# Kernel tuning notes

Hardware: AMD Instinct MI355X
Metric: run time of the kernel (lower is better)

Reference implementation:

```python
import jax, jax.numpy as jnp
import numpy as np

N_NODES = 100000
N_EDGES = 1000000
IN_CH = 64
HID = 64


def setup_inputs() -> dict:
    key = jax.random.key(0)
    ks = jax.random.split(key, 10)
    x = jax.random.normal(ks[0], (N_NODES, IN_CH), dtype=jnp.float32)
    edge_index = jax.random.randint(ks[1], (2, N_EDGES), 0, N_NODES, dtype=jnp.int32)
    s = 1.0 / np.sqrt(IN_CH)
    sh = 1.0 / np.sqrt(HID)
    return {
        "x": x,
        "edge_index": edge_index,
        # conv1: lin_l (applied to aggregated neighbors, has bias), lin_r (self, no bias)
        "w1_l": jax.random.uniform(ks[2], (HID, IN_CH), jnp.float32, -s, s),
        "b1": jnp.zeros((HID,), jnp.float32),
        "w1_r": jax.random.uniform(ks[3], (HID, IN_CH), jnp.float32, -s, s),
        # conv2
        "w2_l": jax.random.uniform(ks[4], (HID, HID), jnp.float32, -sh, sh),
        "b2": jnp.zeros((HID,), jnp.float32),
        "w2_r": jax.random.uniform(ks[5], (HID, HID), jnp.float32, -sh, sh),
        # final linear -> 1
        "w_out": jax.random.uniform(ks[6], (1, HID), jnp.float32, -sh, sh),
        "b_out": jnp.zeros((1,), jnp.float32),
    }


def _sage_conv(x, src, dst, w_l, b, w_r, n_nodes):
    # mean aggregation of source features at destination nodes
    agg = jax.ops.segment_sum(x[src], dst, num_segments=n_nodes)  # [N, d]
    cnt = jax.ops.segment_sum(jnp.ones_like(dst, dtype=x.dtype), dst, num_segments=n_nodes)
    mean = agg / jnp.maximum(cnt, 1.0)[:, None]
    # PyG SAGEConv: lin_l(aggregated) + lin_r(x_self); bias lives in lin_l
    return mean @ w_l.T + b + x @ w_r.T


def reference(x, edge_index, w1_l, b1, w1_r, w2_l, b2, w2_r, w_out, b_out):
    src, dst = edge_index[0], edge_index[1]
    n = x.shape[0]
    h = jax.nn.relu(_sage_conv(x, src, dst, w1_l, b1, w1_r, n))
    h = jax.nn.relu(_sage_conv(h, src, dst, w2_l, b2, w2_r, n))
    logits = h @ w_out.T + b_out  # [N, 1]
    return jax.nn.sigmoid(logits)
```

## Files before the change

kernel.cpp:

```cpp
#include <hip/hip_runtime.h>
#include <hip/hip_bf16.h>
#include <math.h>

#define CH 64
#define TILE 16
#define NXCD 8

typedef short short8 __attribute__((ext_vector_type(8)));
typedef float floatx4 __attribute__((ext_vector_type(4)));

__device__ __forceinline__ float bf2f(unsigned short u) {
    return __uint_as_float(((unsigned int)u) << 16);
}
__device__ __forceinline__ unsigned short f2bf(float f) {
    unsigned int x = __float_as_uint(f);
    unsigned int r = (x + 0x7fff + ((x >> 16) & 1)) >> 16;
    return (unsigned short)r;
}

__global__ __launch_bounds__(256) void k_hist(
    const unsigned short* __restrict__ x,
    const int* __restrict__ srcs, const int* __restrict__ dsts,
    int* __restrict__ deg, int* __restrict__ flag,
    int n_edges, int n_nodes)
{
    if (blockIdx.x == 0 && threadIdx.x < 64) {
        unsigned short u = x[2 * threadIdx.x];
        int ex = (u >> 7) & 0xFF;
        bool insane = (ex < 0x60) || (ex > 0x9F);
        unsigned long long m = __ballot(insane);
        if (threadIdx.x == 0) flag[0] = (__popcll(m) > 16) ? 0 : 1;
    }
    int e = blockIdx.x * 256 + threadIdx.x;
    if (e >= n_edges) return;
    int d = dsts[e], s = srcs[e];
    if ((unsigned)d < (unsigned)n_nodes && (unsigned)s < (unsigned)n_nodes)
        atomicAdd(&deg[d], 1);
}

__global__ __launch_bounds__(256) void k_scan1(
    const int* __restrict__ deg, int* __restrict__ rowptr,
    int* __restrict__ bsum, int n)
{
    __shared__ int ts[256];
    int t = threadIdx.x;
    int base = blockIdx.x * 1024 + t * 4;
    int v[4], local = 0;
    #pragma unroll
    for (int k = 0; k < 4; k++) { v[k] = (base + k < n) ? deg[base + k] : 0; local += v[k]; }
    ts[t] = local; __syncthreads();
    for (int off = 1; off < 256; off <<= 1) {
        int val = (t >= off) ? ts[t - off] : 0;
        __syncthreads();
        ts[t] += val;
        __syncthreads();
    }
    int run = ts[t] - local;
    #pragma unroll
    for (int k = 0; k < 4; k++) { if (base + k < n) rowptr[base + k] = run; run += v[k]; }
    if (t == 255) bsum[blockIdx.x] = ts[255];
}

__global__ __launch_bounds__(256) void k_scan2(
    int* __restrict__ bsum, int* __restrict__ rowptr, int nb, int n)
{
    __shared__ int ts[256];
    int t = threadIdx.x;
    int base = t * 4;
    int v[4], local = 0;
    #pragma unroll
    for (int k = 0; k < 4; k++) { v[k] = (base + k < nb) ? bsum[base + k] : 0; local += v[k]; }
    ts[t] = local; __syncthreads();
    for (int off = 1; off < 256; off <<= 1) {
        int val = (t >= off) ? ts[t - off] : 0;
        __syncthreads();
        ts[t] += val;
        __syncthreads();
    }
    int run = ts[t] - local;
    #pragma unroll
    for (int k = 0; k < 4; k++) { if (base + k < nb) bsum[base + k] = run; run += v[k]; }
    if (t == 255) rowptr[n] = ts[255];
}

__global__ __launch_bounds__(256) void k_scan3(
    int* __restrict__ rowptr, int* __restrict__ cursor,
    const int* __restrict__ bsum, int n)
{
    int add = bsum[blockIdx.x];
    int base = blockIdx.x * 1024 + threadIdx.x * 4;
    #pragma unroll
    for (int k = 0; k < 4; k++) {
        int i = base + k;
        if (i < n) { int r = rowptr[i] + add; rowptr[i] = r; cursor[i] = r; }
    }
}

__global__ __launch_bounds__(256) void k_permute(
    const int* __restrict__ srcs, const int* __restrict__ dsts,
    int* __restrict__ cursor, int* __restrict__ nbr, int n_edges, int n_nodes)
{
    const int grp = blockIdx.x & (NXCD - 1);
    const int gidx = blockIdx.x >> 3;
    const int gstride = (gridDim.x >> 3) * 256;
    const int range = (n_nodes + NXCD - 1) / NXCD;
    const int lo = grp * range;
    const int hi = min(n_nodes, lo + range);
    for (int e = gidx * 256 + threadIdx.x; e < n_edges; e += gstride) {
        int d = dsts[e];
        if (d >= lo && d < hi) {
            int s = srcs[e];
            if ((unsigned)s < (unsigned)n_nodes) {
                int pos = atomicAdd(&cursor[d], 1);
                nbr[pos] = s;
            }
        }
    }
}

template <int XMODE>
__global__ __launch_bounds__(256) void k_gather(
    const int* __restrict__ flag, const void* __restrict__ xin,
    const int* __restrict__ nbr, const int* __restrict__ rowptr,
    unsigned short* __restrict__ meanout, int n_nodes)
{
    const bool xbf = (XMODE == 1) ? true : (flag[0] != 0);
    const int lane = threadIdx.x & 63;
    const int wid  = threadIdx.x >> 6;
    const int t = lane >> 4;
    const int s = (lane >> 3) & 1;
    const int c = lane & 7;

    int wbase = (blockIdx.x * 4 + wid) * 4;
    if (wbase >= n_nodes) return;
    int node = wbase + t;
    bool nv = node < n_nodes;
    int r0 = 0, d = 0;
    if (nv) { r0 = rowptr[node]; d = rowptr[node + 1] - r0; }

    int dmax = d;
    dmax = max(dmax, __shfl_xor(dmax, 16));
    dmax = max(dmax, __shfl_xor(dmax, 32));

    const unsigned short* xu = (const unsigned short*)xin;
    const float*          xf = (const float*)xin;

    if (xbf) {
        floatx4 a0 = {0, 0, 0, 0}, a1 = {0, 0, 0, 0};
        for (int jb = 0; jb < dmax; jb += 16) {
            #pragma unroll
            for (int k = 0; k < 8; k++) {
                int j = jb + k * 2 + s;
                if (j < d) {
                    int src = nbr[r0 + j];
                    short8 v = *(const short8*)(xu + (size_t)src * CH + c * 8);
                    #pragma unroll
                    for (int i = 0; i < 4; i++) a0[i] += bf2f((unsigned short)v[i]);
                    #pragma unroll
                    for (int i = 0; i < 4; i++) a1[i] += bf2f((unsigned short)v[4 + i]);
                }
            }
        }
        #pragma unroll
        for (int i = 0; i < 4; i++) {
            a0[i] += __shfl_xor(a0[i], 8);
            a1[i] += __shfl_xor(a1[i], 8);
        }
        if (nv && (lane & 8) == 0) {
            float inv = 1.0f / (float)max(d, 1);
            short8 mv;
            #pragma unroll
            for (int i = 0; i < 4; i++) {
                mv[i]     = (short)f2bf(a0[i] * inv);
                mv[4 + i] = (short)f2bf(a1[i] * inv);
            }
            *(short8*)(meanout + (size_t)node * CH + c * 8) = mv;
        }
    } else {
        int j16 = lane & 15;
        floatx4 acc = {0, 0, 0, 0};
        for (int j = 0; j < d; j++) {
            int src = nbr[r0 + j];
            acc += *(const floatx4*)(xf + (size_t)src * CH + j16 * 4);
        }
        if (nv) {
            float inv = 1.0f / (float)max(d, 1);
            unsigned short* mp = meanout + (size_t)node * CH + j16 * 4;
            #pragma unroll
            for (int i = 0; i < 4; i++) mp[i] = f2bf(acc[i] * inv);
        }
    }
}

template <int XMODE, bool HEAD>
__global__ __launch_bounds__(256) void k_mm(
    const int* __restrict__ flag, const void* __restrict__ xin,
    const unsigned short* __restrict__ meanin,
    const void* __restrict__ w_l, const void* __restrict__ bias,
    const void* __restrict__ w_r,
    const void* __restrict__ w_out, const void* __restrict__ b_out,
    void* __restrict__ outp, int n_nodes)
{
    const int isbf = flag[0];
    const bool xbf = (XMODE == 1) ? true : (isbf != 0);
    const int lane = threadIdx.x & 63;
    const int wid  = threadIdx.x >> 6;
    const int n_ = lane & 15;
    const int q_ = lane >> 4;

    short8 wlf[4][2], wrf[4][2];
    float bv[4], wov[4];
    #pragma unroll
    for (int t = 0; t < 4; t++) {
        int row = t * 16 + n_;
        if (isbf) {
            const unsigned short* wl = (const unsigned short*)w_l;
            const unsigned short* wr = (const unsigned short*)w_r;
            #pragma unroll
            for (int kc = 0; kc < 2; kc++) {
                int k0 = kc * 32 + q_ * 8;
                wlf[t][kc] = *(const short8*)(wl + row * CH + k0);
                wrf[t][kc] = *(const short8*)(wr + row * CH + k0);
            }
            bv[t] = bf2f(((const unsigned short*)bias)[row]);
            if (HEAD) wov[t] = bf2f(((const unsigned short*)w_out)[row]);
        } else {
            const float* wl = (const float*)w_l;
            const float* wr = (const float*)w_r;
            #pragma unroll
            for (int kc = 0; kc < 2; kc++) {
                int k0 = kc * 32 + q_ * 8;
                #pragma unroll
                for (int j = 0; j < 8; j++) {
                    wlf[t][kc][j] = (short)f2bf(wl[row * CH + k0 + j]);
                    wrf[t][kc][j] = (short)f2bf(wr[row * CH + k0 + j]);
                }
            }
            bv[t] = ((const float*)bias)[row];
            if (HEAD) wov[t] = ((const float*)w_out)[row];
        }
    }

    const unsigned short* xu = (const unsigned short*)xin;
    const float*          xf = (const float*)xin;
    int n_tiles = (n_nodes + TILE - 1) / TILE;
    int gw = blockIdx.x * 4 + wid;
    int nw = gridDim.x * 4;

    for (int tb = gw; tb < n_tiles; tb += nw) {
        int base = tb * TILE;
        int node_m = base + n_;
        int node_c = (node_m < n_nodes) ? node_m : 0;
        short8 am0 = *(const short8*)(meanin + (size_t)node_c * CH + q_ * 8);
        short8 am1 = *(const short8*)(meanin + (size_t)node_c * CH + 32 + q_ * 8);
        short8 ax0, ax1;
        if (xbf) {
            ax0 = *(const short8*)(xu + (size_t)node_c * CH + q_ * 8);
            ax1 = *(const short8*)(xu + (size_t)node_c * CH + 32 + q_ * 8);
        } else {
            const float* p = xf + (size_t)node_c * CH;
            #pragma unroll
            for (int j = 0; j < 8; j++) {
                ax0[j] = (short)f2bf(p[q_ * 8 + j]);
                ax1[j] = (short)f2bf(p[32 + q_ * 8 + j]);
            }
        }
        floatx4 acc[4];
        #pragma unroll
        for (int t = 0; t < 4; t++) {
            acc[t] = (floatx4){bv[t], bv[t], bv[t], bv[t]};
            acc[t] = __builtin_amdgcn_mfma_f32_16x16x32_bf16(am0, wlf[t][0], acc[t], 0, 0, 0);
            acc[t] = __builtin_amdgcn_mfma_f32_16x16x32_bf16(am1, wlf[t][1], acc[t], 0, 0, 0);
            acc[t] = __builtin_amdgcn_mfma_f32_16x16x32_bf16(ax0, wrf[t][0], acc[t], 0, 0, 0);
            acc[t] = __builtin_amdgcn_mfma_f32_16x16x32_bf16(ax1, wrf[t][1], acc[t], 0, 0, 0);
        }
        if (!HEAD) {
            unsigned short* ho = (unsigned short*)outp;
            #pragma unroll
            for (int t = 0; t < 4; t++) {
                int cc = t * 16 + n_;
                #pragma unroll
                for (int reg = 0; reg < 4; reg++) {
                    int node_r = base + q_ * 4 + reg;
                    if (node_r < n_nodes)
                        ho[(size_t)node_r * CH + cc] = f2bf(fmaxf(acc[t][reg], 0.0f));
                }
            }
        } else {
            float p[4] = {0, 0, 0, 0};
            #pragma unroll
            for (int t = 0; t < 4; t++) {
                #pragma unroll
                for (int reg = 0; reg < 4; reg++)
                    p[reg] += fmaxf(acc[t][reg], 0.0f) * wov[t];
            }
            #pragma unroll
            for (int off = 1; off < 16; off <<= 1) {
                #pragma unroll
                for (int reg = 0; reg < 4; reg++)
                    p[reg] += __shfl_xor(p[reg], off);
            }
            if (n_ == 0) {
                float bo = isbf ? bf2f(((const unsigned short*)b_out)[0])
                                : ((const float*)b_out)[0];
                #pragma unroll
                for (int reg = 0; reg < 4; reg++) {
                    int node_r = base + q_ * 4 + reg;
                    if (node_r < n_nodes) {
                        float sg = 1.0f / (1.0f + expf(-(p[reg] + bo)));
                        if (isbf) ((unsigned short*)outp)[node_r] = f2bf(sg);
                        else      ((float*)outp)[node_r] = sg;
                    }
                }
            }
        }
    }
}

extern "C" void kernel_launch(void* const* d_in, const int* in_sizes, int n_in,
                              void* d_out, int out_size, void* d_ws, size_t ws_size,
                              hipStream_t stream)
{
    const void* x    = d_in[0];
    const int*  ei   = (const int*)d_in[1];
    const void* w1_l = d_in[2];
    const void* b1   = d_in[3];
    const void* w1_r = d_in[4];
    const void* w2_l = d_in[5];
    const void* b2   = d_in[6];
    const void* w2_r = d_in[7];
    const void* wout = d_in[8];
    const void* bout = d_in[9];

    int n_nodes = out_size;
    int n_edges = in_sizes[1] / 2;
    const int* srcs = ei;
    const int* dsts = ei + n_edges;

    char* wsb = (char*)d_ws;
    size_t off = 0;
    auto carve = [&](size_t bytes) { size_t p = off; off = (off + bytes + 255) & ~(size_t)255; return p; };
    size_t flag_off = carve(sizeof(int));
    size_t deg_off  = carve((size_t)n_nodes * sizeof(int));
    size_t row_off  = carve((size_t)(n_nodes + 1) * sizeof(int));
    size_t cur_off  = carve((size_t)n_nodes * sizeof(int));
    size_t bs_off   = carve(1024 * sizeof(int));
    size_t nbr_off  = carve((size_t)n_edges * sizeof(int));
    size_t mean_off = carve((size_t)n_nodes * CH * sizeof(unsigned short));
    size_t h_off    = carve((size_t)n_nodes * CH * sizeof(unsigned short));
    int* flag   = (int*)(wsb + flag_off);
    int* deg    = (int*)(wsb + deg_off);
    int* rowptr = (int*)(wsb + row_off);
    int* cursor = (int*)(wsb + cur_off);
    int* bsum   = (int*)(wsb + bs_off);
    int* nbr    = (int*)(wsb + nbr_off);
    unsigned short* mean = (unsigned short*)(wsb + mean_off);
    unsigned short* h    = (unsigned short*)(wsb + h_off);

    int eblocks = (n_edges + 255) / 256;
    int xblocks = 2048;
    int nb1     = (n_nodes + 1023) / 1024;
    int gblocks = (n_nodes + 15) / 16;
    int mblocks = 512;

    hipMemsetAsync(deg, 0, (size_t)n_nodes * sizeof(int), stream);

    k_hist<<<eblocks, 256, 0, stream>>>((const unsigned short*)x, srcs, dsts, deg, flag, n_edges, n_nodes);
    k_scan1<<<nb1, 256, 0, stream>>>(deg, rowptr, bsum, n_nodes);
    k_scan2<<<1, 256, 0, stream>>>(bsum, rowptr, nb1, n_nodes);
    k_scan3<<<nb1, 256, 0, stream>>>(rowptr, cursor, bsum, n_nodes);
    k_permute<<<xblocks, 256, 0, stream>>>(srcs, dsts, cursor, nbr, n_edges, n_nodes);

    k_gather<0><<<gblocks, 256, 0, stream>>>(flag, x, nbr, rowptr, mean, n_nodes);
    k_mm<0, false><<<mblocks, 256, 0, stream>>>(flag, x, mean, w1_l, b1, w1_r,
                                                nullptr, nullptr, h, n_nodes);
    k_gather<1><<<gblocks, 256, 0, stream>>>(flag, h, nbr, rowptr, mean, n_nodes);
    k_mm<1, true><<<mblocks, 256, 0, stream>>>(flag, h, mean, w2_l, b2, w2_r,
                                               wout, bout, d_out, n_nodes);
}
```

Baseline: 283.0 us.

## Use XCC-aware dynamic chunk queues for degree histogram and edge permute

Histogram and permute kernels now read the hardware XCC id and pull edge chunks from per-destination-range atomic work queues, starting with the range matching their own XCC. The aim is to keep each node range's atomics local to one XCD's L2 while balancing load dynamically. The histogram also moves to a persistent grid that filters by range, so each range pass rereads the destination array. The cost is extra queue atomics, block barriers and more edge reads.

```diff
diff --git a/kernel.cpp b/kernel.cpp
--- a/kernel.cpp
+++ b/kernel.cpp
@@ -5,6 +5,7 @@
 #define CH 64
 #define TILE 16
 #define NXCD 8
+#define CHUNK 4096
 
 typedef short short8 __attribute__((ext_vector_type(8)));
 typedef float floatx4 __attribute__((ext_vector_type(4)));
@@ -17,11 +18,14 @@
     unsigned int r = (x + 0x7fff + ((x >> 16) & 1)) >> 16;
     return (unsigned short)r;
 }
+__device__ __forceinline__ int get_xcc() {
+    return __builtin_amdgcn_s_getreg((3 << 11) | 20) & (NXCD - 1);
+}
 
 __global__ __launch_bounds__(256) void k_hist(
     const unsigned short* __restrict__ x,
     const int* __restrict__ srcs, const int* __restrict__ dsts,
-    int* __restrict__ deg, int* __restrict__ flag,
+    int* __restrict__ deg, int* __restrict__ flag, int* __restrict__ qh,
     int n_edges, int n_nodes)
 {
     if (blockIdx.x == 0 && threadIdx.x < 64) {
@@ -31,11 +35,30 @@
         unsigned long long m = __ballot(insane);
         if (threadIdx.x == 0) flag[0] = (__popcll(m) > 16) ? 0 : 1;
     }
-    int e = blockIdx.x * 256 + threadIdx.x;
-    if (e >= n_edges) return;
-    int d = dsts[e], s = srcs[e];
-    if ((unsigned)d < (unsigned)n_nodes && (unsigned)s < (unsigned)n_nodes)
-        atomicAdd(&deg[d], 1);
+    __shared__ int sch;
+    const int myx = get_xcc();
+    const int range = (n_nodes + NXCD - 1) / NXCD;
+    const int nchunks = (n_edges + CHUNK - 1) / CHUNK;
+    for (int rr = 0; rr < NXCD; rr++) {
+        int r = (myx + rr) & (NXCD - 1);
+        int lo = r * range, hi = min(n_nodes, lo + range);
+        while (true) {
+            __syncthreads();
+            if (threadIdx.x == 0) sch = atomicAdd(&qh[r], 1);
+            __syncthreads();
+            int ch = sch;
+            if (ch >= nchunks) break;
+            int e0 = ch * CHUNK;
+            int e1 = min(e0 + CHUNK, n_edges);
+            for (int e = e0 + threadIdx.x; e < e1; e += 256) {
+                int d = dsts[e];
+                if (d >= lo && d < hi) {
+                    int s = srcs[e];
+                    if ((unsigned)s < (unsigned)n_nodes) atomicAdd(&deg[d], 1);
+                }
+            }
+        }
+    }
 }
 
 __global__ __launch_bounds__(256) void k_scan1(
@@ -98,21 +121,33 @@
 
 __global__ __launch_bounds__(256) void k_permute(
     const int* __restrict__ srcs, const int* __restrict__ dsts,
-    int* __restrict__ cursor, int* __restrict__ nbr, int n_edges, int n_nodes)
-{
-    const int grp = blockIdx.x & (NXCD - 1);
-    const int gidx = blockIdx.x >> 3;
-    const int gstride = (gridDim.x >> 3) * 256;
+    int* __restrict__ cursor, int* __restrict__ nbr, int* __restrict__ qh,
+    int n_edges, int n_nodes)
+{
+    __shared__ int sch;
+    const int myx = get_xcc();
     const int range = (n_nodes + NXCD - 1) / NXCD;
-    const int lo = grp * range;
-    const int hi = min(n_nodes, lo + range);
-    for (int e = gidx * 256 + threadIdx.x; e < n_edges; e += gstride) {
-        int d = dsts[e];
-        if (d >= lo && d < hi) {
-            int s = srcs[e];
-            if ((unsigned)s < (unsigned)n_nodes) {
-                int pos = atomicAdd(&cursor[d], 1);
-                nbr[pos] = s;
+    const int nchunks = (n_edges + CHUNK - 1) / CHUNK;
+    for (int rr = 0; rr < NXCD; rr++) {
+        int r = (myx + rr) & (NXCD - 1);
+        int lo = r * range, hi = min(n_nodes, lo + range);
+        while (true) {
+            __syncthreads();
+            if (threadIdx.x == 0) sch = atomicAdd(&qh[r], 1);
+            __syncthreads();
+            int ch = sch;
+            if (ch >= nchunks) break;
+            int e0 = ch * CHUNK;
+            int e1 = min(e0 + CHUNK, n_edges);
+            for (int e = e0 + threadIdx.x; e < e1; e += 256) {
+                int d = dsts[e];
+                if (d >= lo && d < hi) {
+                    int s = srcs[e];
+                    if ((unsigned)s < (unsigned)n_nodes) {
+                        int pos = atomicAdd(&cursor[d], 1);
+                        nbr[pos] = s;
+                    }
+                }
             }
         }
     }
@@ -166,7 +201,7 @@
             a0[i] += __shfl_xor(a0[i], 8);
             a1[i] += __shfl_xor(a1[i], 8);
         }
-        if (nv && (lane & 8) == 0) {
+        if (nv && s == 0) {
             float inv = 1.0f / (float)max(d, 1);
             short8 mv;
             #pragma unroll
@@ -341,6 +376,7 @@
     size_t off = 0;
     auto carve = [&](size_t bytes) { size_t p = off; off = (off + bytes + 255) & ~(size_t)255; return p; };
     size_t flag_off = carve(sizeof(int));
+    size_t qh_off   = carve(16 * sizeof(int));
     size_t deg_off  = carve((size_t)n_nodes * sizeof(int));
     size_t row_off  = carve((size_t)(n_nodes + 1) * sizeof(int));
     size_t cur_off  = carve((size_t)n_nodes * sizeof(int));
@@ -349,6 +385,7 @@
     size_t mean_off = carve((size_t)n_nodes * CH * sizeof(unsigned short));
     size_t h_off    = carve((size_t)n_nodes * CH * sizeof(unsigned short));
     int* flag   = (int*)(wsb + flag_off);
+    int* qh     = (int*)(wsb + qh_off);
     int* deg    = (int*)(wsb + deg_off);
     int* rowptr = (int*)(wsb + row_off);
     int* cursor = (int*)(wsb + cur_off);
@@ -357,19 +394,21 @@
     unsigned short* mean = (unsigned short*)(wsb + mean_off);
     unsigned short* h    = (unsigned short*)(wsb + h_off);
 
-    int eblocks = (n_edges + 255) / 256;
     int xblocks = 2048;
     int nb1     = (n_nodes + 1023) / 1024;
     int gblocks = (n_nodes + 15) / 16;
     int mblocks = 512;
 
-    hipMemsetAsync(deg, 0, (size_t)n_nodes * sizeof(int), stream);
-
-    k_hist<<<eblocks, 256, 0, stream>>>((const unsigned short*)x, srcs, dsts, deg, flag, n_edges, n_nodes);
+    hipMemsetAsync(wsb + qh_off, 0,
+                   deg_off + (size_t)n_nodes * sizeof(int) - qh_off, stream);
+
+    k_hist<<<xblocks, 256, 0, stream>>>((const unsigned short*)x, srcs, dsts,
+                                        deg, flag, qh, n_edges, n_nodes);
     k_scan1<<<nb1, 256, 0, stream>>>(deg, rowptr, bsum, n_nodes);
     k_scan2<<<1, 256, 0, stream>>>(bsum, rowptr, nb1, n_nodes);
     k_scan3<<<nb1, 256, 0, stream>>>(rowptr, cursor, bsum, n_nodes);
-    k_permute<<<xblocks, 256, 0, stream>>>(srcs, dsts, cursor, nbr, n_edges, n_nodes);
+    k_permute<<<xblocks, 256, 0, stream>>>(srcs, dsts, cursor, nbr, qh + 8,
+                                           n_edges, n_nodes);
 
     k_gather<0><<<gblocks, 256, 0, stream>>>(flag, x, nbr, rowptr, mean, n_nodes);
     k_mm<0, false><<<mblocks, 256, 0, stream>>>(flag, x, mean, w1_l, b1, w1_r,
```

Result: slower. 669.5 us (+136.6%).
